# Optimization experiments

Hardware: AMD Instinct MI355X
Metric: run time of the kernel (lower is better)

The kernel has to match this reference:

```python
import jax, jax.numpy as jnp
import numpy as np

B, L, H = 8, 512, 768
W = 5          # max_phrase_len
K = 32         # max_phrases
P = 256        # phrase_dim
EPS = 1e-5
NEG = -1e30


def layernorm(x, g, b):
    m = jnp.mean(x, axis=-1, keepdims=True)
    v = jnp.var(x, axis=-1, keepdims=True)
    return (x - m) * jax.lax.rsqrt(v + EPS) * g + b


def setup_inputs() -> dict:
    key = jax.random.key(0)
    ks = jax.random.split(key, 12)
    s = 0.02
    return {
        "hidden": jax.random.normal(ks[0], (B, L, H), dtype=jnp.float32),
        "attention_mask": jnp.ones((B, L), dtype=jnp.int32),
        # span_scorer: Linear(4H->H), LayerNorm(H), ReLU, Linear(H->1)
        "w1": jax.random.normal(ks[1], (4 * H, H), dtype=jnp.float32) * s,
        "b1": jnp.zeros((H,), dtype=jnp.float32),
        "g1": jnp.ones((H,), dtype=jnp.float32),
        "beta1": jnp.zeros((H,), dtype=jnp.float32),
        "w2": jax.random.normal(ks[2], (H, 1), dtype=jnp.float32) * s,
        "b2": jnp.zeros((1,), dtype=jnp.float32),
        # proj: Linear(H->P)
        "wp": jax.random.normal(ks[3], (H, P), dtype=jnp.float32) * s,
        "bp": jnp.zeros((P,), dtype=jnp.float32),
        # attention_gate: Linear(H->H/2), Tanh, Linear(H/2->1)
        "wg1": jax.random.normal(ks[4], (H, H // 2), dtype=jnp.float32) * s,
        "bg1": jnp.zeros((H // 2,), dtype=jnp.float32),
        "wg2": jax.random.normal(ks[5], (H // 2, 1), dtype=jnp.float32) * s,
        "bg2": jnp.zeros((1,), dtype=jnp.float32),
        # out_norm: LayerNorm(P)
        "gout": jnp.ones((P,), dtype=jnp.float32),
        "bout": jnp.zeros((P,), dtype=jnp.float32),
    }


def reference(hidden, attention_mask, w1, b1, g1, beta1, w2, b2,
              wp, bp, wg1, bg1, wg2, bg2, gout, bout):
    mask = attention_mask.astype(bool)  # [B,L]
    # validity of span (i, j=i+w): all tokens i..i+w in mask and i+w < L
    valids = []
    v = mask
    for w in range(W):
        if w > 0:
            shifted = jnp.pad(mask[:, w:], ((0, 0), (0, w)), constant_values=False)
            v = v & shifted
        valids.append(v)
    valid = jnp.stack(valids, axis=2)  # [B,L,W]

    # span means via prefix sums
    prefix = jnp.pad(jnp.cumsum(hidden, axis=1), ((0, 0), (1, 0), (0, 0)))  # [B,L+1,H]
    i_idx = jnp.arange(L)
    j_idx = jnp.minimum(i_idx[:, None] + jnp.arange(W)[None, :], L - 1)  # [L,W]

    start = hidden[:, :, None, :]                                  # [B,L,1,H]
    end = hidden[:, j_idx]                                         # [B,L,W,H]
    span_sum = prefix[:, j_idx + 1] - prefix[:, i_idx][:, :, None, :]
    mean = span_sum / (jnp.arange(W, dtype=hidden.dtype) + 1.0)[None, None, :, None]
    diff = end - start
    start_b = jnp.broadcast_to(start, end.shape)
    feat = jnp.concatenate([start_b, end, mean, diff], axis=-1)    # [B,L,W,4H]

    h = feat @ w1 + b1
    h = jax.nn.relu(layernorm(h, g1, beta1))                       # dropout is eval-mode identity
    score = (h @ w2 + b2)[..., 0]                                  # [B,L,W]
    score = jnp.where(valid, score, NEG)

    flat_scores = score.reshape(B, L * W)
    top_scores, top_idx = jax.lax.top_k(flat_scores, K)            # [B,K]
    phrase_masks = top_scores > NEG / 2

    mean_flat = mean.reshape(B, L * W, H)
    embs = jnp.take_along_axis(mean_flat, top_idx[..., None], axis=1)  # [B,K,H]
    embs = jnp.where(phrase_masks[..., None], embs, 0.0)               # zero-pad features
    phrase_scores = jnp.where(phrase_masks, top_scores, -10.0)

    ti = top_idx // W
    tw = top_idx % W
    spans = jnp.stack([ti, ti + tw], axis=-1)                      # [B,K,2]
    spans = jnp.where(phrase_masks[..., None], spans, 0)

    gate_logits = (jnp.tanh(embs @ wg1 + bg1) @ wg2 + bg2)[..., 0]  # [B,K]
    gate_logits = jnp.where(phrase_masks, gate_logits, -1e9)
    phrase_attention = jax.nn.softmax(gate_logits, axis=-1)

    phrase_embeds = layernorm(embs @ wp + bp, gout, bout)           # [B,K,P]
    return phrase_embeds, phrase_masks, phrase_attention, phrase_scores, spans
```

## Files before the change

kernel.cpp:

```cpp
#include <hip/hip_runtime.h>
#include <float.h>
#include <math.h>
#include <stdint.h>

#define B_   8
#define L_   512
#define H_   768
#define W_   5
#define K_   32
#define P_   256
#define EPS_ 1e-5f
#define NEG_ -1e30f

typedef _Float16 half8 __attribute__((ext_vector_type(8)));
typedef _Float16 half4v __attribute__((ext_vector_type(4)));
typedef float floatx4 __attribute__((ext_vector_type(4)));

static const size_t OFF_X   = 0;
static const size_t OFF_AH  = 9437184;
static const size_t OFF_AL  = 11010048;
static const size_t OFF_BH  = 12582912;
static const size_t OFF_BL  = 13467648;
static const size_t OFF_SC  = 14352384;
static const size_t OFF_TS  = 14372864;
static const size_t OFF_TI  = 14373120;
static const size_t OFF_GL  = 14373376;
static const size_t OFF_EMB = 14373632;
static const size_t OFF_Y   = 14570240;

#define A_SCALE 8.0f
#define B_SCALE 64.0f
#define INV_SCALE (1.0f / 512.0f)

__global__ __launch_bounds__(256) void prep_kernel(const float* __restrict__ hid,
                                                   const float* __restrict__ w1,
                                                   _Float16* __restrict__ ah,
                                                   _Float16* __restrict__ al,
                                                   _Float16* __restrict__ bh,
                                                   _Float16* __restrict__ bl) {
    __shared__ float ld[64][65];
    if (blockIdx.x < 3072) {
        int idx = (blockIdx.x * 256 + threadIdx.x) * 4;
        float4 x = *(const float4*)(hid + idx);
        float xs[4] = {x.x * A_SCALE, x.y * A_SCALE, x.z * A_SCALE, x.w * A_SCALE};
        half4v h, l;
#pragma unroll
        for (int i = 0; i < 4; ++i) {
            _Float16 hi = (_Float16)xs[i];
            h[i] = hi;
            l[i] = (_Float16)(xs[i] - (float)hi);
        }
        *(half4v*)(ah + idx) = h;
        *(half4v*)(al + idx) = l;
    } else {
        int bid = blockIdx.x - 3072;
        int n0 = (bid / 12) * 64;
        int k0 = (bid % 12) * 64;
        int t = threadIdx.x;
        int rsel = n0 / 768;
        int c0 = n0 - rsel * 768;
#pragma unroll 4
        for (int r = 0; r < 16; ++r) {
            int idx = r * 256 + t;
            int kk = idx >> 6, nn = idx & 63;
            int k = k0 + kk, c = c0 + nn;
            float v;
            if (rsel == 0)      v = w1[(size_t)k * 768 + c] - w1[(size_t)(2304 + k) * 768 + c];
            else if (rsel == 1) v = w1[(size_t)(768 + k) * 768 + c] + w1[(size_t)(2304 + k) * 768 + c];
            else                v = w1[(size_t)(1536 + k) * 768 + c];
            ld[kk][nn] = v * B_SCALE;
        }
        __syncthreads();
#pragma unroll 4
        for (int r = 0; r < 16; ++r) {
            int idx = r * 256 + t;
            int nn = idx >> 6, kk = idx & 63;
            float v = ld[kk][nn];
            _Float16 h = (_Float16)v;
            _Float16 lo = (_Float16)(v - (float)h);
            size_t o = (size_t)(n0 + nn) * 768 + k0 + kk;
            bh[o] = h;
            bl[o] = lo;
        }
    }
}

typedef const __attribute__((address_space(1))) void* gas_ptr;
typedef __attribute__((address_space(3))) void* las_ptr;
__device__ __forceinline__ void async_ld16(const _Float16* g, _Float16* l) {
    __builtin_amdgcn_global_load_lds((gas_ptr)g, (las_ptr)l, 16, 0, 0);
}

__global__ __launch_bounds__(256) void mfma_gemm_kernel(const _Float16* __restrict__ Ah,
                                                        const _Float16* __restrict__ Al,
                                                        const _Float16* __restrict__ Bh,
                                                        const _Float16* __restrict__ Bl,
                                                        float* __restrict__ C) {
    __shared__ _Float16 sAh[2 * 4096];
    __shared__ _Float16 sAl[2 * 4096];
    __shared__ _Float16 sBh[2 * 2048];
    __shared__ _Float16 sBl[2 * 2048];
    int tid = threadIdx.x;
    int lane = tid & 63;
    int wave = tid >> 6;
    int m0 = blockIdx.x * 128, n0 = blockIdx.y * 64;

    const _Float16* src = (wave == 0) ? Ah : (wave == 1) ? Al : (wave == 2) ? Bh : Bl;
    _Float16* dstb = (wave == 0) ? sAh : (wave == 1) ? sAl : (wave == 2) ? sBh : sBl;
    int psz  = (wave < 2) ? 4096 : 2048;
    int nch  = (wave < 2) ? 8 : 4;
    int row0 = (wave < 2) ? m0 : n0;
    int qg = (lane & 3) ^ ((lane >> 3) & 3);
    const _Float16* gp = src + (size_t)(row0 + (lane >> 2)) * 768 + qg * 8;

    int wr = wave >> 1, wc = wave & 1;
    int off_lane = (lane & 15) * 64 + (((lane >> 4) ^ ((lane >> 1) & 3)) * 16);
    floatx4 acc[4][2];
#pragma unroll
    for (int i = 0; i < 4; ++i)
#pragma unroll
        for (int j = 0; j < 2; ++j)
            acc[i][j] = (floatx4){0.f, 0.f, 0.f, 0.f};

#pragma unroll
    for (int c = 0; c < 8; ++c) {
        if (c < nch) async_ld16(gp + (size_t)c * 16 * 768, dstb + c * 512);
    }

    int parity = 0;
    for (int k0 = 0; k0 < 768; k0 += 32) {
        __syncthreads();
        if (k0 + 32 < 768) {
            _Float16* dst = dstb + (parity ^ 1) * psz;
            const _Float16* g = gp + k0 + 32;
#pragma unroll
            for (int c = 0; c < 8; ++c) {
                if (c < nch) async_ld16(g + (size_t)c * 16 * 768, dst + c * 512);
            }
        }

        const char* bAh = (const char*)sAh + parity * 8192 + wr * 4096 + off_lane;
        const char* bAl = (const char*)sAl + parity * 8192 + wr * 4096 + off_lane;
        const char* bBh = (const char*)sBh + parity * 4096 + wc * 2048 + off_lane;
        const char* bBl = (const char*)sBl + parity * 4096 + wc * 2048 + off_lane;
        half8 a_h[4], a_l[4], b_h[2], b_l[2];
#pragma unroll
        for (int i = 0; i < 4; ++i) {
            a_h[i] = *(const half8*)(bAh + i * 1024);
            a_l[i] = *(const half8*)(bAl + i * 1024);
        }
#pragma unroll
        for (int j = 0; j < 2; ++j) {
            b_h[j] = *(const half8*)(bBh + j * 1024);
            b_l[j] = *(const half8*)(bBl + j * 1024);
        }
#pragma unroll
        for (int i = 0; i < 4; ++i)
#pragma unroll
            for (int j = 0; j < 2; ++j) {
                acc[i][j] = __builtin_amdgcn_mfma_f32_16x16x32_f16(a_h[i], b_h[j], acc[i][j], 0, 0, 0);
                acc[i][j] = __builtin_amdgcn_mfma_f32_16x16x32_f16(a_h[i], b_l[j], acc[i][j], 0, 0, 0);
                acc[i][j] = __builtin_amdgcn_mfma_f32_16x16x32_f16(a_l[i], b_h[j], acc[i][j], 0, 0, 0);
            }
        parity ^= 1;
    }

    int colc = lane & 15, quad = lane >> 4;
#pragma unroll
    for (int i = 0; i < 4; ++i) {
#pragma unroll
        for (int r = 0; r < 4; ++r) {
            int row = m0 + wr * 64 + i * 16 + quad * 4 + r;
            float* Cp = C + (size_t)row * 2304 + n0 + wc * 32 + colc;
#pragma unroll
            for (int j = 0; j < 2; ++j)
                Cp[j * 16] = acc[i][j][r] * INV_SCALE;
        }
    }
}

__global__ __launch_bounds__(256) void score_kernel(const float* __restrict__ X,
                                                    const int* __restrict__ mask,
                                                    const float* __restrict__ b1,
                                                    const float* __restrict__ g1,
                                                    const float* __restrict__ beta1,
                                                    const float* __restrict__ w2,
                                                    const float* __restrict__ b2,
                                                    float* __restrict__ scores) {
    int wave = threadIdx.x >> 6;
    int lane = threadIdx.x & 63;
    int bi = blockIdx.x * 4 + wave;
    int b = bi >> 9, i = bi & 511;

    float4 a[3], b1c[3], g1c[3], btc[3], w2c[3], ss[3], e[3];
    const float4* Xrow = (const float4*)(X + (size_t)bi * 2304);
#pragma unroll
    for (int q = 0; q < 3; ++q) {
        int f = lane + q * 64;
        a[q]   = Xrow[f];
        b1c[q] = ((const float4*)b1)[f];
        g1c[q] = ((const float4*)g1)[f];
        btc[q] = ((const float4*)beta1)[f];
        w2c[q] = ((const float4*)w2)[f];
        ss[q]  = make_float4(0.f, 0.f, 0.f, 0.f);
    }
    float bias2 = b2[0];
    int jcur = i - 1;
    float sc_loc[W_];

    for (int w = 0; w < W_; ++w) {
        int j = min(i + w, 511);
        const float4* Xj = (const float4*)(X + (size_t)(b * 512 + j) * 2304);
        if (j > jcur) {
#pragma unroll
            for (int q = 0; q < 3; ++q) {
                int f = lane + q * 64;
                float4 cc = Xj[384 + f];
                ss[q].x += cc.x; ss[q].y += cc.y; ss[q].z += cc.z; ss[q].w += cc.w;
                e[q] = Xj[192 + f];
            }
            jcur = j;
        }
        float invw = 1.0f / (float)(w + 1);
        float4 h[3];
        float psum = 0.f;
#pragma unroll
        for (int q = 0; q < 3; ++q) {
            h[q].x = a[q].x + e[q].x + ss[q].x * invw + b1c[q].x;
            h[q].y = a[q].y + e[q].y + ss[q].y * invw + b1c[q].y;
            h[q].z = a[q].z + e[q].z + ss[q].z * invw + b1c[q].z;
            h[q].w = a[q].w + e[q].w + ss[q].w * invw + b1c[q].w;
            psum += h[q].x + h[q].y + h[q].z + h[q].w;
        }
#pragma unroll
        for (int m = 1; m < 64; m <<= 1) psum += __shfl_xor(psum, m, 64);
        float mean = psum * (1.f / 768.f);

        float pv = 0.f;
#pragma unroll
        for (int q = 0; q < 3; ++q) {
            float dx = h[q].x - mean, dy = h[q].y - mean, dz = h[q].z - mean, dw = h[q].w - mean;
            pv += dx * dx + dy * dy + dz * dz + dw * dw;
        }
#pragma unroll
        for (int m = 1; m < 64; m <<= 1) pv += __shfl_xor(pv, m, 64);
        float rstd = rsqrtf(pv * (1.f / 768.f) + EPS_);

        float pd = 0.f;
#pragma unroll
        for (int q = 0; q < 3; ++q) {
            float yx = fmaxf((h[q].x - mean) * rstd * g1c[q].x + btc[q].x, 0.f);
            float yy = fmaxf((h[q].y - mean) * rstd * g1c[q].y + btc[q].y, 0.f);
            float yz = fmaxf((h[q].z - mean) * rstd * g1c[q].z + btc[q].z, 0.f);
            float yw = fmaxf((h[q].w - mean) * rstd * g1c[q].w + btc[q].w, 0.f);
            pd += yx * w2c[q].x + yy * w2c[q].y + yz * w2c[q].z + yw * w2c[q].w;
        }
#pragma unroll
        for (int m = 1; m < 64; m <<= 1) pd += __shfl_xor(pd, m, 64);
        sc_loc[w] = pd + bias2;
    }

    if (lane < W_) {
        int w = lane;
        bool ok = (i + w) < 512;
        if (ok) {
            for (int t = 0; t <= w; ++t) ok = ok && (mask[b * 512 + i + t] != 0);
        }
        scores[b * 2560 + i * 5 + w] = ok ? sc_loc[w] : NEG_;
    }
}

__device__ __forceinline__ uint64_t shfl_xor_u64(uint64_t x, int m) {
    uint32_t lo = (uint32_t)x, hi = (uint32_t)(x >> 32);
    lo = (uint32_t)__shfl_xor((int)lo, m, 64);
    hi = (uint32_t)__shfl_xor((int)hi, m, 64);
    return ((uint64_t)hi << 32) | lo;
}

__global__ __launch_bounds__(256) void topk_kernel(const float* __restrict__ scores,
                                                   float* __restrict__ tops,
                                                   int* __restrict__ topi,
                                                   float* __restrict__ out_masks,
                                                   float* __restrict__ out_scores,
                                                   float* __restrict__ out_spans) {
    int b = blockIdx.x;
    int tid = threadIdx.x;
    int lane = tid & 63;
    int wv = tid >> 6;
    __shared__ uint64_t lists[256 * 9];
    __shared__ uint64_t wmax[4];
    __shared__ uint64_t gS;

    uint64_t v[10];
#pragma unroll
    for (int q = 0; q < 10; ++q) {
        int t = q * 256 + tid;
        float f = scores[b * 2560 + t];
        uint32_t bits = __float_as_uint(f);
        uint32_t mk = bits ^ ((bits & 0x80000000u) ? 0xFFFFFFFFu : 0x80000000u);
        v[q] = ((uint64_t)mk << 32) | (uint64_t)(0xFFFFFFFFu - (uint32_t)t);
    }
#pragma unroll
    for (int p = 0; p < 5; ++p) {
#pragma unroll
        for (int i = 0; i < 9; i += 2) {
            if (v[i] < v[i + 1]) { uint64_t t = v[i]; v[i] = v[i + 1]; v[i + 1] = t; }
        }
#pragma unroll
        for (int i = 1; i < 9; i += 2) {
            if (v[i] < v[i + 1]) { uint64_t t = v[i]; v[i] = v[i + 1]; v[i + 1] = t; }
        }
    }
#pragma unroll
    for (int j = 0; j < 9; ++j) lists[tid * 9 + j] = v[j + 1];
    uint64_t my = v[0];
    int h = 0;

    for (int k = 0; k < K_; ++k) {
        uint64_t m = my;
#pragma unroll
        for (int s = 1; s < 64; s <<= 1) {
            uint64_t o = shfl_xor_u64(m, s);
            if (o > m) m = o;
        }
        if (lane == 0) wmax[wv] = m;
        __syncthreads();
        if (tid == 0) {
            uint64_t g = wmax[0];
#pragma unroll
            for (int q = 1; q < 4; ++q) if (wmax[q] > g) g = wmax[q];
            gS = g;
            uint32_t mk = (uint32_t)(g >> 32);
            uint32_t bits = mk ^ ((mk & 0x80000000u) ? 0x80000000u : 0xFFFFFFFFu);
            float tv = __uint_as_float(bits);
            int tix = (int)(0xFFFFFFFFu - (uint32_t)(g & 0xFFFFFFFFu));
            tops[b * 32 + k] = tv;
            topi[b * 32 + k] = tix;
            bool mm = tv > (NEG_ * 0.5f);
            out_masks[b * 32 + k] = mm ? 1.0f : 0.0f;
            out_scores[b * 32 + k] = mm ? tv : -10.0f;
            int tI = tix / 5, tw = tix % 5;
            out_spans[(b * 32 + k) * 2 + 0] = mm ? (float)tI : 0.0f;
            out_spans[(b * 32 + k) * 2 + 1] = mm ? (float)(tI + tw) : 0.0f;
        }
        __syncthreads();
        uint64_t g = gS;
        if (my == g) {
            my = (h < 9) ? lists[tid * 9 + h] : 0ull;
            ++h;
        }
    }
}

__global__ __launch_bounds__(256) void gather_emb_kernel(const float* __restrict__ hidden,
                                                         const float* __restrict__ tops,
                                                         const int* __restrict__ topi,
                                                         float* __restrict__ Embs) {
    int bk = blockIdx.x;
    int b = bk >> 5;
    int tid = threadIdx.x;
    int idx = topi[bk];
    bool valid = tops[bk] > (NEG_ * 0.5f);
    int tI = idx / 5, tw = idx % 5;
    int jend = min(tI + tw, L_ - 1);
    float inv = 1.0f / (float)(tw + 1);
#pragma unroll
    for (int q = 0; q < 3; ++q) {
        int c = tid + q * 256;
        float s = 0.f;
        if (valid) {
            for (int l = tI; l <= jend; ++l) s += hidden[(size_t)(b * 512 + l) * 768 + c];
            s *= inv;
        }
        Embs[(size_t)bk * 768 + c] = s;
    }
}

__global__ __launch_bounds__(256) void phrase_gemm_kernel(const float* __restrict__ Embs,
                                                          const float* __restrict__ wg1,
                                                          const float* __restrict__ bg1,
                                                          const float* __restrict__ wp,
                                                          const float* __restrict__ bp,
                                                          float* __restrict__ Y) {
    __shared__ float As[32][34];
    __shared__ float Bs[32][64];
    int tid = threadIdx.x;
    int m0 = blockIdx.x * 32;
    int cn0 = blockIdx.y * 64;
    const float* Wp; const float* biasp; int ldw;
    if (cn0 < 384) { Wp = wg1 + cn0;        biasp = bg1 + cn0;        ldw = 384; }
    else           { Wp = wp + (cn0 - 384); biasp = bp + (cn0 - 384); ldw = 256; }

    int tx = tid & 15;
    int ty = tid >> 4;
    int ar = tid >> 3, akq = (tid & 7) * 4;
    int bk = tid >> 3, bcq = (tid & 7) * 8;
    float acc[2][4] = {};

    for (int k0 = 0; k0 < 768; k0 += 32) {
        float4 av  = *(const float4*)(Embs + (size_t)(m0 + ar) * 768 + k0 + akq);
        float4 bv0 = *(const float4*)(Wp + (size_t)(k0 + bk) * ldw + bcq);
        float4 bv1 = *(const float4*)(Wp + (size_t)(k0 + bk) * ldw + bcq + 4);
        __syncthreads();
        As[akq + 0][ar] = av.x;
        As[akq + 1][ar] = av.y;
        As[akq + 2][ar] = av.z;
        As[akq + 3][ar] = av.w;
        *(float4*)&Bs[bk][bcq]     = bv0;
        *(float4*)&Bs[bk][bcq + 4] = bv1;
        __syncthreads();
#pragma unroll
        for (int kk = 0; kk < 32; ++kk) {
            float2 a = *(const float2*)&As[kk][ty * 2];
            float4 b = *(const float4*)&Bs[kk][tx * 4];
            acc[0][0] += a.x * b.x; acc[0][1] += a.x * b.y; acc[0][2] += a.x * b.z; acc[0][3] += a.x * b.w;
            acc[1][0] += a.y * b.x; acc[1][1] += a.y * b.y; acc[1][2] += a.y * b.z; acc[1][3] += a.y * b.w;
        }
    }
#pragma unroll
    for (int i = 0; i < 2; ++i) {
        float* Yp = Y + (size_t)(m0 + ty * 2 + i) * 640 + cn0 + tx * 4;
        float4 o = make_float4(acc[i][0] + biasp[tx * 4 + 0], acc[i][1] + biasp[tx * 4 + 1],
                               acc[i][2] + biasp[tx * 4 + 2], acc[i][3] + biasp[tx * 4 + 3]);
        *(float4*)Yp = o;
    }
}

__global__ __launch_bounds__(256) void phrase_post_kernel(const float* __restrict__ Y,
                                                          const float* __restrict__ wg2,
                                                          const float* __restrict__ bg2,
                                                          const float* __restrict__ tops,
                                                          const float* __restrict__ gout,
                                                          const float* __restrict__ bout,
                                                          float* __restrict__ gate,
                                                          float* __restrict__ out_embeds) {
    int wv = threadIdx.x >> 6, lane = threadIdx.x & 63;
    int row = blockIdx.x * 4 + wv;
    const float* Yrow = Y + (size_t)row * 640;

    float s = 0.f;
#pragma unroll
    for (int q = 0; q < 6; ++q) {
        int c = lane + q * 64;
        s += tanhf(Yrow[c]) * wg2[c];
    }
#pragma unroll
    for (int m = 1; m < 64; m <<= 1) s += __shfl_xor(s, m, 64);
    if (lane == 0) {
        bool valid = tops[row] > (NEG_ * 0.5f);
        gate[row] = valid ? (s + bg2[0]) : -1e9f;
    }

    float4 p = *(const float4*)(Yrow + 384 + lane * 4);
    float sm = p.x + p.y + p.z + p.w;
#pragma unroll
    for (int m = 1; m < 64; m <<= 1) sm += __shfl_xor(sm, m, 64);
    float mean = sm * (1.f / 256.f);
    float dx = p.x - mean, dy = p.y - mean, dz = p.z - mean, dw = p.w - mean;
    float v = dx * dx + dy * dy + dz * dz + dw * dw;
#pragma unroll
    for (int m = 1; m < 64; m <<= 1) v += __shfl_xor(v, m, 64);
    float rstd = rsqrtf(v * (1.f / 256.f) + EPS_);
    int c = lane * 4;
    float4 o;
    o.x = dx * rstd * gout[c]     + bout[c];
    o.y = dy * rstd * gout[c + 1] + bout[c + 1];
    o.z = dz * rstd * gout[c + 2] + bout[c + 2];
    o.w = dw * rstd * gout[c + 3] + bout[c + 3];
    *(float4*)(out_embeds + (size_t)row * 256 + c) = o;
}

__global__ void attn_kernel(const float* __restrict__ gate, float* __restrict__ out_attn) {
    int b = threadIdx.x;
    if (b < 8) {
        float mx = -FLT_MAX;
        for (int k = 0; k < 32; ++k) mx = fmaxf(mx, gate[b * 32 + k]);
        float e[32];
        float s = 0.f;
        for (int k = 0; k < 32; ++k) { e[k] = expf(gate[b * 32 + k] - mx); s += e[k]; }
        float inv = 1.f / s;
        for (int k = 0; k < 32; ++k) out_attn[b * 32 + k] = e[k] * inv;
    }
}

extern "C" void kernel_launch(void* const* d_in, const int* in_sizes, int n_in,
                              void* d_out, int out_size, void* d_ws, size_t ws_size,
                              hipStream_t stream) {
    const float* hidden = (const float*)d_in[0];
    const int*   amask  = (const int*)d_in[1];
    const float* w1     = (const float*)d_in[2];
    const float* b1     = (const float*)d_in[3];
    const float* g1     = (const float*)d_in[4];
    const float* beta1  = (const float*)d_in[5];
    const float* w2     = (const float*)d_in[6];
    const float* b2     = (const float*)d_in[7];
    const float* wp     = (const float*)d_in[8];
    const float* bp     = (const float*)d_in[9];
    const float* wg1    = (const float*)d_in[10];
    const float* bg1    = (const float*)d_in[11];
    const float* wg2    = (const float*)d_in[12];
    const float* bg2    = (const float*)d_in[13];
    const float* gout   = (const float*)d_in[14];
    const float* bout   = (const float*)d_in[15];

    float* ws = (float*)d_ws;
    float*     X    = ws + OFF_X;
    _Float16*  ah   = (_Float16*)(ws + OFF_AH);
    _Float16*  al   = (_Float16*)(ws + OFF_AL);
    _Float16*  bh   = (_Float16*)(ws + OFF_BH);
    _Float16*  bl   = (_Float16*)(ws + OFF_BL);
    float*     sc   = ws + OFF_SC;
    float*     ts   = ws + OFF_TS;
    int*       ti   = (int*)(ws + OFF_TI);
    float*     gl   = ws + OFF_GL;
    float*     Embs = ws + OFF_EMB;
    float*     Y    = ws + OFF_Y;

    float* out = (float*)d_out;
    float* out_embeds = out;
    float* out_masks  = out + 65536;
    float* out_attn   = out + 65792;
    float* out_scores = out + 66048;
    float* out_spans  = out + 66304;

    prep_kernel<<<3504, 256, 0, stream>>>(hidden, w1, ah, al, bh, bl);
    mfma_gemm_kernel<<<dim3(32, 36), 256, 0, stream>>>(ah, al, bh, bl, X);
    score_kernel<<<1024, 256, 0, stream>>>(X, amask, b1, g1, beta1, w2, b2, sc);
    topk_kernel<<<8, 256, 0, stream>>>(sc, ts, ti, out_masks, out_scores, out_spans);
    gather_emb_kernel<<<256, 256, 0, stream>>>(hidden, ts, ti, Embs);
    phrase_gemm_kernel<<<dim3(8, 10), 256, 0, stream>>>(Embs, wg1, bg1, wp, bp, Y);
    phrase_post_kernel<<<64, 256, 0, stream>>>(Y, wg2, bg2, ts, gout, bout, gl, out_embeds);
    attn_kernel<<<1, 64, 0, stream>>>(gl, out_attn);
}
```

Measured before the change: 236.3 us.

## Widen GEMM tile, stage span rows in LDS, fuse softmax into post kernel

The main MFMA GEMM tile grows from 128x64 to 128x128, so each wave computes a 64x64 sub-tile and the grid drops to 32x18. This raises operand reuse per LDS load but doubles accumulator registers and leaves half as many blocks, which may hurt occupancy. The score kernel now loads the shared window of neighbouring token rows into LDS once per block, so the four waves no longer each re-read them from global memory. The separate single-block softmax kernel is merged into the phrase post kernel (one block per batch), which removes a launch but runs that kernel on only 8 blocks.

```diff
diff --git a/kernel.cpp b/kernel.cpp
--- a/kernel.cpp
+++ b/kernel.cpp
@@ -24,7 +24,6 @@
 static const size_t OFF_SC  = 14352384;
 static const size_t OFF_TS  = 14372864;
 static const size_t OFF_TI  = 14373120;
-static const size_t OFF_GL  = 14373376;
 static const size_t OFF_EMB = 14373632;
 static const size_t OFF_Y   = 14570240;
 
@@ -98,66 +97,59 @@
                                                         float* __restrict__ C) {
     __shared__ _Float16 sAh[2 * 4096];
     __shared__ _Float16 sAl[2 * 4096];
-    __shared__ _Float16 sBh[2 * 2048];
-    __shared__ _Float16 sBl[2 * 2048];
+    __shared__ _Float16 sBh[2 * 4096];
+    __shared__ _Float16 sBl[2 * 4096];
     int tid = threadIdx.x;
     int lane = tid & 63;
     int wave = tid >> 6;
-    int m0 = blockIdx.x * 128, n0 = blockIdx.y * 64;
+    int m0 = blockIdx.x * 128, n0 = blockIdx.y * 128;
 
     const _Float16* src = (wave == 0) ? Ah : (wave == 1) ? Al : (wave == 2) ? Bh : Bl;
     _Float16* dstb = (wave == 0) ? sAh : (wave == 1) ? sAl : (wave == 2) ? sBh : sBl;
-    int psz  = (wave < 2) ? 4096 : 2048;
-    int nch  = (wave < 2) ? 8 : 4;
     int row0 = (wave < 2) ? m0 : n0;
     int qg = (lane & 3) ^ ((lane >> 3) & 3);
     const _Float16* gp = src + (size_t)(row0 + (lane >> 2)) * 768 + qg * 8;
 
     int wr = wave >> 1, wc = wave & 1;
     int off_lane = (lane & 15) * 64 + (((lane >> 4) ^ ((lane >> 1) & 3)) * 16);
-    floatx4 acc[4][2];
+    floatx4 acc[4][4];
 #pragma unroll
     for (int i = 0; i < 4; ++i)
 #pragma unroll
-        for (int j = 0; j < 2; ++j)
+        for (int j = 0; j < 4; ++j)
             acc[i][j] = (floatx4){0.f, 0.f, 0.f, 0.f};
 
 #pragma unroll
-    for (int c = 0; c < 8; ++c) {
-        if (c < nch) async_ld16(gp + (size_t)c * 16 * 768, dstb + c * 512);
-    }
+    for (int c = 0; c < 8; ++c)
+        async_ld16(gp + (size_t)c * 16 * 768, dstb + c * 512);
 
     int parity = 0;
     for (int k0 = 0; k0 < 768; k0 += 32) {
         __syncthreads();
         if (k0 + 32 < 768) {
-            _Float16* dst = dstb + (parity ^ 1) * psz;
+            _Float16* dst = dstb + (parity ^ 1) * 4096;
             const _Float16* g = gp + k0 + 32;
 #pragma unroll
-            for (int c = 0; c < 8; ++c) {
-                if (c < nch) async_ld16(g + (size_t)c * 16 * 768, dst + c * 512);
-            }
+            for (int c = 0; c < 8; ++c)
+                async_ld16(g + (size_t)c * 16 * 768, dst + c * 512);
         }
 
         const char* bAh = (const char*)sAh + parity * 8192 + wr * 4096 + off_lane;
         const char* bAl = (const char*)sAl + parity * 8192 + wr * 4096 + off_lane;
-        const char* bBh = (const char*)sBh + parity * 4096 + wc * 2048 + off_lane;
-        const char* bBl = (const char*)sBl + parity * 4096 + wc * 2048 + off_lane;
-        half8 a_h[4], a_l[4], b_h[2], b_l[2];
+        const char* bBh = (const char*)sBh + parity * 8192 + wc * 4096 + off_lane;
+        const char* bBl = (const char*)sBl + parity * 8192 + wc * 4096 + off_lane;
+        half8 a_h[4], a_l[4], b_h[4], b_l[4];
 #pragma unroll
         for (int i = 0; i < 4; ++i) {
             a_h[i] = *(const half8*)(bAh + i * 1024);
             a_l[i] = *(const half8*)(bAl + i * 1024);
-        }
-#pragma unroll
-        for (int j = 0; j < 2; ++j) {
-            b_h[j] = *(const half8*)(bBh + j * 1024);
-            b_l[j] = *(const half8*)(bBl + j * 1024);
+            b_h[i] = *(const half8*)(bBh + i * 1024);
+            b_l[i] = *(const half8*)(bBl + i * 1024);
         }
 #pragma unroll
         for (int i = 0; i < 4; ++i)
 #pragma unroll
-            for (int j = 0; j < 2; ++j) {
+            for (int j = 0; j < 4; ++j) {
                 acc[i][j] = __builtin_amdgcn_mfma_f32_16x16x32_f16(a_h[i], b_h[j], acc[i][j], 0, 0, 0);
                 acc[i][j] = __builtin_amdgcn_mfma_f32_16x16x32_f16(a_h[i], b_l[j], acc[i][j], 0, 0, 0);
                 acc[i][j] = __builtin_amdgcn_mfma_f32_16x16x32_f16(a_l[i], b_h[j], acc[i][j], 0, 0, 0);
@@ -171,9 +163,9 @@
 #pragma unroll
         for (int r = 0; r < 4; ++r) {
             int row = m0 + wr * 64 + i * 16 + quad * 4 + r;
-            float* Cp = C + (size_t)row * 2304 + n0 + wc * 32 + colc;
-#pragma unroll
-            for (int j = 0; j < 2; ++j)
+            float* Cp = C + (size_t)row * 2304 + n0 + wc * 64 + colc;
+#pragma unroll
+            for (int j = 0; j < 4; ++j)
                 Cp[j * 16] = acc[i][j][r] * INV_SCALE;
         }
     }
@@ -187,12 +179,25 @@
                                                     const float* __restrict__ w2,
                                                     const float* __restrict__ b2,
                                                     float* __restrict__ scores) {
-    int wave = threadIdx.x >> 6;
-    int lane = threadIdx.x & 63;
-    int bi = blockIdx.x * 4 + wave;
-    int b = bi >> 9, i = bi & 511;
-
-    float4 a[3], b1c[3], g1c[3], btc[3], w2c[3], ss[3], e[3];
+    __shared__ float sE[8 * 768];
+    __shared__ float sC[8 * 768];
+    int tid = threadIdx.x;
+    int wv = tid >> 6, lane = tid & 63;
+    int bi0 = blockIdx.x * 4;
+    int b = bi0 >> 9, i0 = bi0 & 511;
+
+#pragma unroll
+    for (int u0 = 0; u0 < 6; ++u0) {
+        int u = u0 * 256 + tid;
+        int t = u / 192, f = u - t * 192;
+        int j = min(i0 + t, 511);
+        const float4* Xj = (const float4*)(X + (size_t)(b * 512 + j) * 2304);
+        ((float4*)sE)[t * 192 + f] = Xj[192 + f];
+        ((float4*)sC)[t * 192 + f] = Xj[384 + f];
+    }
+
+    int i = i0 + wv, bi = bi0 + wv;
+    float4 a[3], b1c[3], g1c[3], btc[3], w2c[3], ss[3];
     const float4* Xrow = (const float4*)(X + (size_t)bi * 2304);
 #pragma unroll
     for (int q = 0; q < 3; ++q) {
@@ -205,19 +210,22 @@
         ss[q]  = make_float4(0.f, 0.f, 0.f, 0.f);
     }
     float bias2 = b2[0];
+    __syncthreads();
+
     int jcur = i - 1;
+    float4 e[3];
     float sc_loc[W_];
 
     for (int w = 0; w < W_; ++w) {
         int j = min(i + w, 511);
-        const float4* Xj = (const float4*)(X + (size_t)(b * 512 + j) * 2304);
         if (j > jcur) {
+            int slot = j - i0;
 #pragma unroll
             for (int q = 0; q < 3; ++q) {
                 int f = lane + q * 64;
-                float4 cc = Xj[384 + f];
+                float4 cc = ((const float4*)sC)[slot * 192 + f];
                 ss[q].x += cc.x; ss[q].y += cc.y; ss[q].z += cc.z; ss[q].w += cc.w;
-                e[q] = Xj[192 + f];
+                e[q] = ((const float4*)sE)[slot * 192 + f];
             }
             jcur = j;
         }
@@ -432,54 +440,59 @@
                                                           const float* __restrict__ tops,
                                                           const float* __restrict__ gout,
                                                           const float* __restrict__ bout,
-                                                          float* __restrict__ gate,
+                                                          float* __restrict__ out_attn,
                                                           float* __restrict__ out_embeds) {
+    int b = blockIdx.x;
     int wv = threadIdx.x >> 6, lane = threadIdx.x & 63;
-    int row = blockIdx.x * 4 + wv;
-    const float* Yrow = Y + (size_t)row * 640;
-
-    float s = 0.f;
-#pragma unroll
-    for (int q = 0; q < 6; ++q) {
-        int c = lane + q * 64;
-        s += tanhf(Yrow[c]) * wg2[c];
-    }
-#pragma unroll
-    for (int m = 1; m < 64; m <<= 1) s += __shfl_xor(s, m, 64);
-    if (lane == 0) {
-        bool valid = tops[row] > (NEG_ * 0.5f);
-        gate[row] = valid ? (s + bg2[0]) : -1e9f;
-    }
-
-    float4 p = *(const float4*)(Yrow + 384 + lane * 4);
-    float sm = p.x + p.y + p.z + p.w;
-#pragma unroll
-    for (int m = 1; m < 64; m <<= 1) sm += __shfl_xor(sm, m, 64);
-    float mean = sm * (1.f / 256.f);
-    float dx = p.x - mean, dy = p.y - mean, dz = p.z - mean, dw = p.w - mean;
-    float v = dx * dx + dy * dy + dz * dz + dw * dw;
-#pragma unroll
-    for (int m = 1; m < 64; m <<= 1) v += __shfl_xor(v, m, 64);
-    float rstd = rsqrtf(v * (1.f / 256.f) + EPS_);
-    int c = lane * 4;
-    float4 o;
-    o.x = dx * rstd * gout[c]     + bout[c];
-    o.y = dy * rstd * gout[c + 1] + bout[c + 1];
-    o.z = dz * rstd * gout[c + 2] + bout[c + 2];
-    o.w = dw * rstd * gout[c + 3] + bout[c + 3];
-    *(float4*)(out_embeds + (size_t)row * 256 + c) = o;
-}
-
-__global__ void attn_kernel(const float* __restrict__ gate, float* __restrict__ out_attn) {
-    int b = threadIdx.x;
-    if (b < 8) {
-        float mx = -FLT_MAX;
-        for (int k = 0; k < 32; ++k) mx = fmaxf(mx, gate[b * 32 + k]);
-        float e[32];
+    __shared__ float sgate[32];
+
+    for (int rr = 0; rr < 8; ++rr) {
+        int krow = wv * 8 + rr;
+        int row = b * 32 + krow;
+        const float* Yrow = Y + (size_t)row * 640;
+
         float s = 0.f;
-        for (int k = 0; k < 32; ++k) { e[k] = expf(gate[b * 32 + k] - mx); s += e[k]; }
-        float inv = 1.f / s;
-        for (int k = 0; k < 32; ++k) out_attn[b * 32 + k] = e[k] * inv;
+#pragma unroll
+        for (int q = 0; q < 6; ++q) {
+            int c = lane + q * 64;
+            s += tanhf(Yrow[c]) * wg2[c];
+        }
+#pragma unroll
+        for (int m = 1; m < 64; m <<= 1) s += __shfl_xor(s, m, 64);
+        if (lane == 0) {
+            bool valid = tops[row] > (NEG_ * 0.5f);
+            sgate[krow] = valid ? (s + bg2[0]) : -1e9f;
+        }
+
+        float4 p = *(const float4*)(Yrow + 384 + lane * 4);
+        float sm = p.x + p.y + p.z + p.w;
+#pragma unroll
+        for (int m = 1; m < 64; m <<= 1) sm += __shfl_xor(sm, m, 64);
+        float mean = sm * (1.f / 256.f);
+        float dx = p.x - mean, dy = p.y - mean, dz = p.z - mean, dw = p.w - mean;
+        float v = dx * dx + dy * dy + dz * dz + dw * dw;
+#pragma unroll
+        for (int m = 1; m < 64; m <<= 1) v += __shfl_xor(v, m, 64);
+        float rstd = rsqrtf(v * (1.f / 256.f) + EPS_);
+        int c = lane * 4;
+        float4 o;
+        o.x = dx * rstd * gout[c]     + bout[c];
+        o.y = dy * rstd * gout[c + 1] + bout[c + 1];
+        o.z = dz * rstd * gout[c + 2] + bout[c + 2];
+        o.w = dw * rstd * gout[c + 3] + bout[c + 3];
+        *(float4*)(out_embeds + (size_t)row * 256 + c) = o;
+    }
+    __syncthreads();
+    if (threadIdx.x < 32) {
+        float g = sgate[threadIdx.x];
+        float mx = g;
+#pragma unroll
+        for (int m = 1; m < 32; m <<= 1) mx = fmaxf(mx, __shfl_xor(mx, m, 64));
+        float e = expf(g - mx);
+        float sum = e;
+#pragma unroll
+        for (int m = 1; m < 32; m <<= 1) sum += __shfl_xor(sum, m, 64);
+        out_attn[b * 32 + threadIdx.x] = e / sum;
     }
 }
 
@@ -512,7 +525,6 @@
     float*     sc   = ws + OFF_SC;
     float*     ts   = ws + OFF_TS;
     int*       ti   = (int*)(ws + OFF_TI);
-    float*     gl   = ws + OFF_GL;
     float*     Embs = ws + OFF_EMB;
     float*     Y    = ws + OFF_Y;
 
@@ -524,11 +536,10 @@
     float* out_spans  = out + 66304;
 
     prep_kernel<<<3504, 256, 0, stream>>>(hidden, w1, ah, al, bh, bl);
-    mfma_gemm_kernel<<<dim3(32, 36), 256, 0, stream>>>(ah, al, bh, bl, X);
+    mfma_gemm_kernel<<<dim3(32, 18), 256, 0, stream>>>(ah, al, bh, bl, X);
     score_kernel<<<1024, 256, 0, stream>>>(X, amask, b1, g1, beta1, w2, b2, sc);
     topk_kernel<<<8, 256, 0, stream>>>(sc, ts, ti, out_masks, out_scores, out_spans);
     gather_emb_kernel<<<256, 256, 0, stream>>>(hidden, ts, ti, Embs);
     phrase_gemm_kernel<<<dim3(8, 10), 256, 0, stream>>>(Embs, wg1, bg1, wp, bp, Y);
-    phrase_post_kernel<<<64, 256, 0, stream>>>(Y, wg2, bg2, ts, gout, bout, gl, out_embeds);
-    attn_kernel<<<1, 64, 0, stream>>>(gl, out_attn);
-}
+    phrase_post_kernel<<<8, 256, 0, stream>>>(Y, wg2, bg2, ts, gout, bout, out_attn, out_embeds);
+}
```

Result: slower. 252.0 us (+6.6%).
